# Kernel tuning notes

Hardware: AMD Instinct MI355X
Metric: run time of the kernel (lower is better)

Reference implementation:

```python
import jax, jax.numpy as jnp
import numpy as np

N_NODES = 100000

def setup_inputs() -> dict:
    key = jax.random.key(0)
    k1, k2, k3 = jax.random.split(key, 3)
    x = jax.random.normal(k1, (N_NODES, 64), dtype=jnp.float32)
    edge_index = jax.random.randint(k2, (2, 1600000), 0, N_NODES, dtype=jnp.int64)
    edge_weights = jax.random.uniform(k3, (1600000,), dtype=jnp.float32)
    weight = jnp.ones((1,), dtype=jnp.float32)  # MyConv.weight, reset to 1
    return {"x": x, "edge_index": edge_index, "edge_weights": edge_weights, "weight": weight}

def reference(x, edge_index, edge_weights, weight):
    src = edge_index[0]  # x_j (source nodes, messages flow source->target)
    dst = edge_index[1]  # aggregation target i
    # message: edge_weight * x_j ; aggregate: scatter-add at dst
    msgs = edge_weights[:, None] * x[src]              # [E, D]
    agg = jax.ops.segment_sum(msgs, dst, num_segments=N_NODES)  # [N, D]
    # conv1: x + weight * aggregate, then relu (Encoder only applies conv1)
    return jax.nn.relu(x + weight * agg)
```

## Files before the change

kernel.cpp:

```cpp
#include <hip/hip_runtime.h>

constexpr int N_NODES = 100000;
constexpr int D       = 64;
constexpr int N_EDGES = 1600000;
constexpr int OUT_N4  = N_NODES * D / 4;

constexpr int NPB   = 128;
constexpr int NBUCK = (N_NODES + NPB - 1) / NPB;
constexpr int BCAP  = 2560;
constexpr int CPAD  = 32;
constexpr int PTHREADS = 1024;
constexpr int EPT   = 4;
constexpr int CHUNK = PTHREADS * EPT;
constexpr int PB    = (N_EDGES + CHUNK - 1) / CHUNK;

__global__ void detect_kernel(const unsigned long long* __restrict__ ei,
                              int* __restrict__ flag) {
    if (blockIdx.x == 0 && threadIdx.x == 0) {
        int is64 = 1;
#pragma unroll
        for (int i = 0; i < 8; ++i)
            if (ei[i] >= (unsigned long long)N_NODES) is64 = 0;
        *flag = is64;
    }
}

__device__ __forceinline__ int load_idx(const void* ei_raw, int flag, long long pos) {
    if (flag) return (int)((const long long*)ei_raw)[pos];
    return ((const int*)ei_raw)[pos];
}

__device__ __forceinline__ unsigned short bf16rne(float f) {
    unsigned u = __float_as_uint(f);
    unsigned r = (u + 0x7fffu + ((u >> 16) & 1u)) >> 16;
    return (unsigned short)r;
}
__device__ __forceinline__ float bf16f(unsigned short u) {
    return __uint_as_float(((unsigned)u) << 16);
}

__global__ void prep_kernel(const float4* __restrict__ x4,
                            ushort4* __restrict__ x16v,
                            int* __restrict__ cursor) {
    int i = blockIdx.x * blockDim.x + threadIdx.x;
    int stride = gridDim.x * blockDim.x;
    for (int j = i; j < NBUCK * CPAD; j += stride) cursor[j] = 0;
    for (; i < OUT_N4; i += stride) {
        float4 v = x4[i];
        ushort4 o;
        o.x = bf16rne(v.x); o.y = bf16rne(v.y);
        o.z = bf16rne(v.z); o.w = bf16rne(v.w);
        x16v[i] = o;
    }
}

__global__ __launch_bounds__(PTHREADS) void part_kernel(
        const void* __restrict__ ei_raw,
        const float* __restrict__ ew,
        const int* __restrict__ flag,
        int* __restrict__ cursor,
        int2* __restrict__ slots) {
    __shared__ int  hist[NBUCK];
    __shared__ int  scn[PTHREADS];
    __shared__ int  localbase[NBUCK];
    __shared__ int  runbase[NBUCK];
    __shared__ int  fill[NBUCK];
    __shared__ int2 srt[CHUNK];
    __shared__ unsigned short aux[CHUNK];

    int tid = threadIdx.x;
    for (int t = tid; t < NBUCK; t += PTHREADS) { hist[t] = 0; fill[t] = 0; }
    __syncthreads();

    int f = *flag;
    long long base = (long long)blockIdx.x * CHUNK;

    int  rb[EPT];
    int2 rrec[EPT];
#pragma unroll
    for (int it = 0; it < EPT; ++it) {
        long long e = base + it * PTHREADS + tid;
        if (e < N_EDGES) {
            int src = load_idx(ei_raw, f, e);
            int dst = load_idx(ei_raw, f, (long long)N_EDGES + e);
            int b = dst >> 7;
            rb[it] = b;
            rrec[it].x = (src << 7) | (dst & (NPB - 1));
            rrec[it].y = __float_as_int(ew[e]);
            atomicAdd(&hist[b], 1);
        } else {
            rb[it] = -1;
        }
    }
    __syncthreads();

    scn[tid] = (tid < NBUCK) ? hist[tid] : 0;
    __syncthreads();
    for (int off = 1; off < PTHREADS; off <<= 1) {
        int v = (tid >= off) ? scn[tid - off] : 0;
        __syncthreads();
        scn[tid] += v;
        __syncthreads();
    }
    if (tid < NBUCK) {
        localbase[tid] = scn[tid] - hist[tid];
        int c = hist[tid];
        runbase[tid] = (c > 0) ? atomicAdd(&cursor[tid * CPAD], c) : 0;
    }
    __syncthreads();

#pragma unroll
    for (int it = 0; it < EPT; ++it) {
        int b = rb[it];
        if (b >= 0) {
            int p = localbase[b] + atomicAdd(&fill[b], 1);
            srt[p] = rrec[it];
            aux[p] = (unsigned short)b;
        }
    }
    __syncthreads();

    int total = scn[NBUCK - 1];
    for (int i = tid; i < total; i += PTHREADS) {
        int b = aux[i];
        int g = runbase[b] + (i - localbase[b]);
        if (g < (int)((long long)b * BCAP + BCAP) - (int)((long long)b * BCAP)) {}
        long long gpos = (long long)b * BCAP + g;
        if (g < BCAP) slots[gpos] = srt[i];
    }
}

__global__ __launch_bounds__(256) void sort_bucket_kernel(
        const int* __restrict__ cursor,
        const int2* __restrict__ slots,
        int2* __restrict__ sorted,
        int2* __restrict__ oc ) {
    __shared__ int  hist[NPB];
    __shared__ int  scn[NPB];
    __shared__ int  fill[NPB];
    __shared__ int2 raw[BCAP];
    __shared__ int2 srt[BCAP];

    int tid = threadIdx.x;
    int b   = blockIdx.x;

    if (tid < NPB) { hist[tid] = 0; fill[tid] = 0; }
    __syncthreads();

    int cnt = cursor[b * CPAD];
    if (cnt > BCAP) cnt = BCAP;
    const int2* sb = slots + (long long)b * BCAP;

    for (int i = tid; i < cnt; i += 256) {
        int2 r = sb[i];
        raw[i] = r;
        atomicAdd(&hist[r.x & (NPB - 1)], 1);
    }
    __syncthreads();

    if (tid < NPB) scn[tid] = hist[tid];
    __syncthreads();
    for (int off = 1; off < NPB; off <<= 1) {
        int v = 0;
        if (tid < NPB && tid >= off) v = scn[tid - off];
        __syncthreads();
        if (tid < NPB) scn[tid] += v;
        __syncthreads();
    }

    if (tid < NPB) {
        int node = b * NPB + tid;
        if (node < N_NODES) {
            int2 v;
            v.x = b * BCAP + (scn[tid] - hist[tid]);
            v.y = hist[tid];
            oc[node] = v;
        }
    }
    __syncthreads();

    for (int i = tid; i < cnt; i += 256) {
        int2 r = raw[i];
        int dl = r.x & (NPB - 1);
        int pos = (scn[dl] - hist[dl]) + atomicAdd(&fill[dl], 1);
        srt[pos] = r;
    }
    __syncthreads();

    int2* ob = sorted + (long long)b * BCAP;
    for (int i = tid; i < cnt; i += 256) ob[i] = srt[i];
}

__global__ __launch_bounds__(256) void gather_csr_kernel(
        const unsigned short* __restrict__ x16,
        const int2* __restrict__ oc,
        const int2* __restrict__ sorted,
        const float* __restrict__ weight,
        float* __restrict__ out) {
    int lane = threadIdx.x & 63;
    int node = __builtin_amdgcn_readfirstlane(
        (int)((blockIdx.x * blockDim.x + threadIdx.x) >> 6));
    if (node >= N_NODES) return;

    int2 v = oc[node];
    int beg = __builtin_amdgcn_readfirstlane(v.x);
    int cnt = __builtin_amdgcn_readfirstlane(v.y);
    const int2* s = sorted + beg;

    float a0 = 0.f, a1 = 0.f, a2 = 0.f, a3 = 0.f;
    int k = 0;
    for (; k + 8 <= cnt; k += 8) {
        int2 r0 = s[k];     int2 r1 = s[k + 1];
        int2 r2 = s[k + 2]; int2 r3 = s[k + 3];
        int2 r4 = s[k + 4]; int2 r5 = s[k + 5];
        int2 r6 = s[k + 6]; int2 r7 = s[k + 7];
        float x0 = bf16f(x16[(r0.x >> 7) * D + lane]);
        float x1 = bf16f(x16[(r1.x >> 7) * D + lane]);
        float x2 = bf16f(x16[(r2.x >> 7) * D + lane]);
        float x3 = bf16f(x16[(r3.x >> 7) * D + lane]);
        float x4 = bf16f(x16[(r4.x >> 7) * D + lane]);
        float x5 = bf16f(x16[(r5.x >> 7) * D + lane]);
        float x6 = bf16f(x16[(r6.x >> 7) * D + lane]);
        float x7 = bf16f(x16[(r7.x >> 7) * D + lane]);
        a0 += __int_as_float(r0.y) * x0;
        a1 += __int_as_float(r1.y) * x1;
        a2 += __int_as_float(r2.y) * x2;
        a3 += __int_as_float(r3.y) * x3;
        a0 += __int_as_float(r4.y) * x4;
        a1 += __int_as_float(r5.y) * x5;
        a2 += __int_as_float(r6.y) * x6;
        a3 += __int_as_float(r7.y) * x7;
    }
    for (; k + 2 <= cnt; k += 2) {
        int2 r0 = s[k];
        int2 r1 = s[k + 1];
        a0 += __int_as_float(r0.y) * bf16f(x16[(r0.x >> 7) * D + lane]);
        a1 += __int_as_float(r1.y) * bf16f(x16[(r1.x >> 7) * D + lane]);
    }
    if (k < cnt) {
        int2 r0 = s[k];
        a0 += __int_as_float(r0.y) * bf16f(x16[(r0.x >> 7) * D + lane]);
    }
    float acc = (a0 + a1) + (a2 + a3);

    float r = bf16f(x16[node * D + lane]) + weight[0] * acc;
    out[node * D + lane] = fmaxf(r, 0.f);
}

__global__ void init_out_kernel(const float4* __restrict__ x4,
                                float4* __restrict__ out4) {
    int i = blockIdx.x * blockDim.x + threadIdx.x;
    int stride = gridDim.x * blockDim.x;
    for (; i < OUT_N4; i += stride) out4[i] = x4[i];
}

__global__ __launch_bounds__(256) void scatter_atomic_kernel(
        const float* __restrict__ x,
        const void* __restrict__ ei_raw,
        const float* __restrict__ ew,
        const float* __restrict__ weight,
        const int* __restrict__ flag,
        float* __restrict__ out) {
    long long gid = (long long)blockIdx.x * blockDim.x + threadIdx.x;
    int e = (int)(gid >> 6);
    int d = (int)(gid & 63);
    if (e >= N_EDGES) return;
    int f = *flag;
    int src = load_idx(ei_raw, f, e);
    int dst = load_idx(ei_raw, f, (long long)N_EDGES + e);
    float w = weight[0] * ew[e];
    atomicAdd(&out[dst * D + d], w * x[src * D + d]);
}

__global__ void relu_kernel(float4* __restrict__ out4) {
    int i = blockIdx.x * blockDim.x + threadIdx.x;
    int stride = gridDim.x * blockDim.x;
    for (; i < OUT_N4; i += stride) {
        float4 v = out4[i];
        v.x = fmaxf(v.x, 0.0f);
        v.y = fmaxf(v.y, 0.0f);
        v.z = fmaxf(v.z, 0.0f);
        v.w = fmaxf(v.w, 0.0f);
        out4[i] = v;
    }
}

extern "C" void kernel_launch(void* const* d_in, const int* in_sizes, int n_in,
                              void* d_out, int out_size, void* d_ws, size_t ws_size,
                              hipStream_t stream) {
    const float* x      = (const float*)d_in[0];
    const void*  ei     = d_in[1];
    const float* ew     = (const float*)d_in[2];
    const float* weight = (const float*)d_in[3];
    float* out = (float*)d_out;

    char* w = (char*)d_ws;
    auto align256 = [](size_t v) { return (v + 255) & ~(size_t)255; };

    size_t off = 0;
    int* flag = (int*)(w + off);        off = align256(off + 4);
    int* cursor = (int*)(w + off);      off = align256(off + (size_t)NBUCK * CPAD * 4);
    int2* oc = (int2*)(w + off);        off = align256(off + (size_t)N_NODES * 8);
    unsigned short* x16 = (unsigned short*)(w + off);
                                        off = align256(off + (size_t)N_NODES * D * 2);
    int2* slots = (int2*)(w + off);     off = align256(off + (size_t)NBUCK * BCAP * 8);
    int2* sorted = (int2*)(w + off);    off = align256(off + (size_t)NBUCK * BCAP * 8);
    size_t needed = off;

    detect_kernel<<<1, 64, 0, stream>>>((const unsigned long long*)ei, flag);

    if (ws_size >= needed) {
        prep_kernel<<<2048, 256, 0, stream>>>((const float4*)x, (ushort4*)x16, cursor);
        part_kernel<<<PB, PTHREADS, 0, stream>>>(ei, ew, flag, cursor, slots);
        sort_bucket_kernel<<<NBUCK, 256, 0, stream>>>(cursor, slots, sorted, oc);
        gather_csr_kernel<<<(N_NODES * 64 + 255) / 256, 256, 0, stream>>>(
            x16, oc, sorted, weight, out);
    } else {
        init_out_kernel<<<2048, 256, 0, stream>>>((const float4*)x, (float4*)out);
        long long total = (long long)N_EDGES * 64;
        scatter_atomic_kernel<<<(int)((total + 255) / 256), 256, 0, stream>>>(
            x, ei, ew, weight, flag, out);
        relu_kernel<<<2048, 256, 0, stream>>>((float4*)out);
    }
}
```

Before: 98.48 us.

## Split wavefront into 8 edge groups with 16-byte bf16 row loads in gather

The CSR gather kernel now splits each 64-lane wavefront into 8 row groups of 8 lanes. Each lane loads 8 bf16 features with one 16-byte load and handles two edges per iteration, so 16 edges are in flight per step. Partial sums are combined with xor shuffles, and only the first group writes the output as float4 stores. This aims to cut the number of narrow 2-byte gather loads and raise memory-level parallelism, at the cost of extra shuffle reductions, masked lanes when a node has few edges, and only 8 active lanes in the epilogue.

```diff
diff --git a/kernel.cpp b/kernel.cpp
--- a/kernel.cpp
+++ b/kernel.cpp
@@ -34,9 +34,6 @@
     unsigned u = __float_as_uint(f);
     unsigned r = (u + 0x7fffu + ((u >> 16) & 1u)) >> 16;
     return (unsigned short)r;
-}
-__device__ __forceinline__ float bf16f(unsigned short u) {
-    return __uint_as_float(((unsigned)u) << 16);
 }
 
 __global__ void prep_kernel(const float4* __restrict__ x4,
@@ -124,9 +121,7 @@
     for (int i = tid; i < total; i += PTHREADS) {
         int b = aux[i];
         int g = runbase[b] + (i - localbase[b]);
-        if (g < (int)((long long)b * BCAP + BCAP) - (int)((long long)b * BCAP)) {}
-        long long gpos = (long long)b * BCAP + g;
-        if (g < BCAP) slots[gpos] = srt[i];
+        if (g < BCAP) slots[(long long)b * BCAP + g] = srt[i];
     }
 }
 
@@ -134,7 +129,7 @@
         const int* __restrict__ cursor,
         const int2* __restrict__ slots,
         int2* __restrict__ sorted,
-        int2* __restrict__ oc ) {
+        int2* __restrict__ oc) {
     __shared__ int  hist[NPB];
     __shared__ int  scn[NPB];
     __shared__ int  fill[NPB];
@@ -198,6 +193,8 @@
         const float* __restrict__ weight,
         float* __restrict__ out) {
     int lane = threadIdx.x & 63;
+    int rg   = lane >> 3;
+    int dg   = lane & 7;
     int node = __builtin_amdgcn_readfirstlane(
         (int)((blockIdx.x * blockDim.x + threadIdx.x) >> 6));
     if (node >= N_NODES) return;
@@ -207,44 +204,54 @@
     int cnt = __builtin_amdgcn_readfirstlane(v.y);
     const int2* s = sorted + beg;
 
-    float a0 = 0.f, a1 = 0.f, a2 = 0.f, a3 = 0.f;
-    int k = 0;
-    for (; k + 8 <= cnt; k += 8) {
-        int2 r0 = s[k];     int2 r1 = s[k + 1];
-        int2 r2 = s[k + 2]; int2 r3 = s[k + 3];
-        int2 r4 = s[k + 4]; int2 r5 = s[k + 5];
-        int2 r6 = s[k + 6]; int2 r7 = s[k + 7];
-        float x0 = bf16f(x16[(r0.x >> 7) * D + lane]);
-        float x1 = bf16f(x16[(r1.x >> 7) * D + lane]);
-        float x2 = bf16f(x16[(r2.x >> 7) * D + lane]);
-        float x3 = bf16f(x16[(r3.x >> 7) * D + lane]);
-        float x4 = bf16f(x16[(r4.x >> 7) * D + lane]);
-        float x5 = bf16f(x16[(r5.x >> 7) * D + lane]);
-        float x6 = bf16f(x16[(r6.x >> 7) * D + lane]);
-        float x7 = bf16f(x16[(r7.x >> 7) * D + lane]);
-        a0 += __int_as_float(r0.y) * x0;
-        a1 += __int_as_float(r1.y) * x1;
-        a2 += __int_as_float(r2.y) * x2;
-        a3 += __int_as_float(r3.y) * x3;
-        a0 += __int_as_float(r4.y) * x4;
-        a1 += __int_as_float(r5.y) * x5;
-        a2 += __int_as_float(r6.y) * x6;
-        a3 += __int_as_float(r7.y) * x7;
-    }
-    for (; k + 2 <= cnt; k += 2) {
-        int2 r0 = s[k];
-        int2 r1 = s[k + 1];
-        a0 += __int_as_float(r0.y) * bf16f(x16[(r0.x >> 7) * D + lane]);
-        a1 += __int_as_float(r1.y) * bf16f(x16[(r1.x >> 7) * D + lane]);
-    }
-    if (k < cnt) {
-        int2 r0 = s[k];
-        a0 += __int_as_float(r0.y) * bf16f(x16[(r0.x >> 7) * D + lane]);
-    }
-    float acc = (a0 + a1) + (a2 + a3);
-
-    float r = bf16f(x16[node * D + lane]) + weight[0] * acc;
-    out[node * D + lane] = fmaxf(r, 0.f);
+    float acc[8];
+#pragma unroll
+    for (int j = 0; j < 8; ++j) acc[j] = 0.f;
+
+    for (int k = 0; k < cnt; k += 16) {
+        int iA = k + rg;
+        int iB = iA + 8;
+        int2 rA = s[iA < cnt ? iA : 0];
+        int2 rB = s[iB < cnt ? iB : 0];
+        float wA = (iA < cnt) ? __int_as_float(rA.y) : 0.f;
+        float wB = (iB < cnt) ? __int_as_float(rB.y) : 0.f;
+        uint4 xa = *(const uint4*)(x16 + (rA.x >> 7) * D + dg * 8);
+        uint4 xb = *(const uint4*)(x16 + (rB.x >> 7) * D + dg * 8);
+#pragma unroll
+        for (int j = 0; j < 4; ++j) {
+            unsigned ua = ((const unsigned*)&xa)[j];
+            acc[2 * j]     += wA * __uint_as_float(ua << 16);
+            acc[2 * j + 1] += wA * __uint_as_float(ua & 0xffff0000u);
+        }
+#pragma unroll
+        for (int j = 0; j < 4; ++j) {
+            unsigned ub = ((const unsigned*)&xb)[j];
+            acc[2 * j]     += wB * __uint_as_float(ub << 16);
+            acc[2 * j + 1] += wB * __uint_as_float(ub & 0xffff0000u);
+        }
+    }
+
+#pragma unroll
+    for (int j = 0; j < 8; ++j) {
+        acc[j] += __shfl_xor(acc[j], 8, 64);
+        acc[j] += __shfl_xor(acc[j], 16, 64);
+        acc[j] += __shfl_xor(acc[j], 32, 64);
+    }
+
+    if (rg == 0) {
+        float W = weight[0];
+        uint4 xs = *(const uint4*)(x16 + node * D + dg * 8);
+        float o[8];
+#pragma unroll
+        for (int j = 0; j < 4; ++j) {
+            unsigned us = ((const unsigned*)&xs)[j];
+            o[2 * j]     = fmaxf(__uint_as_float(us << 16)         + W * acc[2 * j],     0.f);
+            o[2 * j + 1] = fmaxf(__uint_as_float(us & 0xffff0000u) + W * acc[2 * j + 1], 0.f);
+        }
+        float4* po = (float4*)(out + node * D + dg * 8);
+        po[0] = make_float4(o[0], o[1], o[2], o[3]);
+        po[1] = make_float4(o[4], o[5], o[6], o[7]);
+    }
 }
 
 __global__ void init_out_kernel(const float4* __restrict__ x4,
```

Result: faster. 94.22 us (-4.3%).
